# Optimization experiments

Hardware: AMD Instinct MI355X
Metric: run time of the kernel (lower is better)

The kernel has to match this reference:

```python
import jax, jax.numpy as jnp
import numpy as np

SIZES = (32, 64, 128, 256, 512)
RATIOS = (0.5, 1.0, 2.0)
STRIDE = 4
H = W = 256
IMG = 1024.0
NMS_THRESH = 0.7
MIN_SIZE = 1.0
BBOX_XFORM_CLIP = float(np.log(1000.0 / 16.0))
NEG = -1e9


def _make_anchors():
    # generate_anchors: ratio-major, scale-minor ordering, centered, rounded
    scales = np.asarray(SIZES, np.float32)
    ratios = np.asarray(RATIOS, np.float32)
    h_r = np.sqrt(ratios)
    w_r = 1.0 / h_r
    ws = (w_r[:, None] * scales[None, :]).reshape(-1)
    hs = (h_r[:, None] * scales[None, :]).reshape(-1)
    base = np.round(np.stack([-ws, -hs, ws, hs], axis=1) / 2.0)  # [A,4]
    # grid_anchors: (y,x)-major shifts, anchors innermost
    sx = np.arange(W, dtype=np.float32) * STRIDE
    sy = np.arange(H, dtype=np.float32) * STRIDE
    yy, xx = np.meshgrid(sy, sx, indexing="ij")
    shifts = np.stack([xx.ravel(), yy.ravel(), xx.ravel(), yy.ravel()], 1)  # [H*W,4]
    return (shifts[:, None, :] + base[None, :, :]).reshape(-1, 4).astype(np.float32)


def setup_inputs() -> dict:
    key = jax.random.key(0)
    k1, k2 = jax.random.split(key)
    N, A = 8, len(SIZES) * len(RATIOS)
    objectness = jax.random.normal(k1, (N, A, H, W), jnp.float32)
    box_regression = jax.random.normal(k2, (N, A * 4, H, W), jnp.float32) * 0.5
    anchors = jnp.asarray(_make_anchors())  # [H*W*A, 4]
    return {"objectness": objectness, "box_regression": box_regression,
            "anchors": anchors, "pre_nms_top_n": 2000}


def _decode(deltas, anchors):
    # BoxCoder.decode_single with weights (1,1,1,1)
    w = anchors[:, 2] - anchors[:, 0]
    h = anchors[:, 3] - anchors[:, 1]
    cx = anchors[:, 0] + 0.5 * w
    cy = anchors[:, 1] + 0.5 * h
    dx, dy = deltas[:, 0], deltas[:, 1]
    dw = jnp.minimum(deltas[:, 2], BBOX_XFORM_CLIP)
    dh = jnp.minimum(deltas[:, 3], BBOX_XFORM_CLIP)
    pcx = dx * w + cx
    pcy = dy * h + cy
    pw = jnp.exp(dw) * w
    ph = jnp.exp(dh) * h
    return jnp.stack([pcx - 0.5 * pw, pcy - 0.5 * ph,
                      pcx + 0.5 * pw, pcy + 0.5 * ph], axis=1)


def _nms_keep(boxes, thresh):
    # boxes [K,4] sorted by descending score; greedy NMS via fixed fori_loop
    x1, y1, x2, y2 = boxes[:, 0], boxes[:, 1], boxes[:, 2], boxes[:, 3]
    area = (x2 - x1) * (y2 - y1)
    lt = jnp.maximum(boxes[:, None, :2], boxes[None, :, :2])
    rb = jnp.minimum(boxes[:, None, 2:], boxes[None, :, 2:])
    wh = jnp.clip(rb - lt, 0.0)
    inter = wh[..., 0] * wh[..., 1]
    iou = inter / (area[:, None] + area[None, :] - inter)
    K = boxes.shape[0]
    rng = jnp.arange(K)

    def body(i, keep):
        sup = keep[i] & (iou[i] > thresh) & (rng > i)
        return keep & ~sup

    return jax.lax.fori_loop(0, K, body, jnp.ones((K,), bool))


def reference(objectness, box_regression, anchors, pre_nms_top_n):
    N, A, Hf, Wf = objectness.shape
    # permute_and_flatten: [N,A,H,W] -> [N, H*W*A] (h,w-major, anchor-minor)
    scores = objectness.transpose(0, 2, 3, 1).reshape(N, -1)
    deltas = (box_regression.reshape(N, A, 4, Hf, Wf)
              .transpose(0, 3, 4, 1, 2).reshape(N, -1, 4))
    proposals = jax.vmap(lambda d: _decode(d, anchors))(deltas)  # [N,M,4]
    # clip_boxes_to_image
    bx = jnp.clip(proposals[..., 0::2], 0.0, IMG)
    by = jnp.clip(proposals[..., 1::2], 0.0, IMG)
    proposals = jnp.stack([bx[..., 0], by[..., 0], bx[..., 1], by[..., 1]], -1)
    probs = jax.nn.sigmoid(scores)
    # remove_small_boxes (mask with -inf score instead of dynamic filter)
    valid = ((proposals[..., 2] - proposals[..., 0]) >= MIN_SIZE) & \
            ((proposals[..., 3] - proposals[..., 1]) >= MIN_SIZE)
    probs = jnp.where(valid, probs, NEG)
    top_scores, top_idx = jax.lax.top_k(probs, pre_nms_top_n)  # [N,K]
    top_boxes = jnp.take_along_axis(proposals, top_idx[..., None], axis=1)
    keep = jax.vmap(lambda b: _nms_keep(b, NMS_THRESH))(top_boxes)  # [N,K] bool
    kf = keep.astype(top_boxes.dtype)
    return jnp.concatenate([top_boxes * kf[..., None],
                            (top_scores * kf)[..., None]], axis=-1)  # [N,K,5]
```

## Files before the change

kernel.cpp:

```cpp
#include <hip/hip_runtime.h>
#include <stdint.h>

#define N_    8
#define A_    15
#define H_    256
#define W_    256
#define M_    (A_*H_*W_)
#define BINS  8192
#define BSH   19
#define KMAJ  3200
#define CAP   8192
#define CBUF  2048
#define WPR   32

__device__ __constant__ double CLIP_  = 4.135166556742356;
__device__ __constant__ double IMG_   = 1024.0;
__device__ __constant__ double MINSZ_ = 1.0;
__device__ __constant__ double NMST_  = 0.7;

__device__ __forceinline__ uint32_t ord32(float s) {
    uint32_t u = __float_as_uint(s);
    return u ^ (uint32_t)(((int32_t)u >> 31) | 0x80000000u);
}

__device__ __forceinline__ void decode_box(
    const float* __restrict__ breg, const float* __restrict__ anchors,
    int n, int a, int hw, int m,
    double& x1, double& y1, double& x2, double& y2)
{
    size_t bbase = ((size_t)(n*60 + a*4)) * 65536 + (size_t)hw;
    double d0 = (double)breg[bbase];
    double d1 = (double)breg[bbase + 65536];
    double d2 = (double)breg[bbase + 2*65536];
    double d3 = (double)breg[bbase + 3*65536];
    float4 av = *reinterpret_cast<const float4*>(anchors + (size_t)m*4);
    double a0 = (double)av.x, a1 = (double)av.y, a2 = (double)av.z, a3 = (double)av.w;
    double ww = a2 - a0, hh = a3 - a1;
    double cx = a0 + 0.5*ww, cy = a1 + 0.5*hh;
    double dw = fmin(d2, CLIP_), dh = fmin(d3, CLIP_);
    double pcx = d0*ww + cx, pcy = d1*hh + cy;
    double pw = exp(dw)*ww, ph = exp(dh)*hh;
    x1 = pcx - 0.5*pw; y1 = pcy - 0.5*ph;
    x2 = pcx + 0.5*pw; y2 = pcy + 0.5*ph;
    x1 = fmin(fmax(x1, 0.0), IMG_);
    y1 = fmin(fmax(y1, 0.0), IMG_);
    x2 = fmin(fmax(x2, 0.0), IMG_);
    y2 = fmin(fmax(y2, 0.0), IMG_);
}

__global__ void k_hist(const float* __restrict__ obj, unsigned int* __restrict__ hist)
{
    __shared__ unsigned int lh[BINS];
    const int n = blockIdx.y;
    for (int i = threadIdx.x; i < BINS; i += blockDim.x) lh[i] = 0;
    __syncthreads();
    const float4* objq = (const float4*)(obj + (size_t)n * M_);
    for (int it = 0; it < 32; ++it) {
        int q = blockIdx.x * 8192 + it * 256 + threadIdx.x;
        float4 v = objq[q];
        atomicAdd(&lh[ord32(v.x) >> BSH], 1u);
        atomicAdd(&lh[ord32(v.y) >> BSH], 1u);
        atomicAdd(&lh[ord32(v.z) >> BSH], 1u);
        atomicAdd(&lh[ord32(v.w) >> BSH], 1u);
    }
    __syncthreads();
    for (int i = threadIdx.x; i < BINS; i += blockDim.x) {
        unsigned int c = lh[i];
        if (c) atomicAdd(&hist[n*BINS + i], c);
    }
}

__global__ void k_findT(const unsigned int* __restrict__ hist, unsigned int* __restrict__ T)
{
    __shared__ unsigned int csum[256];
    const int n = blockIdx.x;
    const int tid = threadIdx.x;
    unsigned int s = 0;
    int hi = BINS - 1 - tid*32;
    for (int i = 0; i < 32; ++i) s += hist[n*BINS + hi - i];
    csum[tid] = s;
    __syncthreads();
    if (tid == 0) {
        unsigned int cum = 0; int c = 0;
        for (; c < 256; ++c) { if (cum + csum[c] >= (unsigned)KMAJ) break; cum += csum[c]; }
        if (c == 256) { T[n] = 0; return; }
        int hi2 = BINS - 1 - c*32;
        unsigned int cum2 = cum; int b = hi2;
        for (int i = 0; i < 32; ++i) {
            b = hi2 - i;
            cum2 += hist[n*BINS + b];
            if (cum2 >= (unsigned)KMAJ) break;
        }
        if (cum2 > (unsigned)CAP && b < BINS-1) b = b + 1;
        T[n] = (unsigned int)b;
    }
}

__global__ void k_collect(const float* __restrict__ obj, const float* __restrict__ breg,
                          const float* __restrict__ anchors, const unsigned int* __restrict__ T,
                          unsigned int* __restrict__ cnt, uint64_t* __restrict__ cand)
{
    __shared__ uint64_t buf[CBUF];
    __shared__ unsigned int lcnt, gbase;
    const int n = blockIdx.y;
    const unsigned int Tn = T[n];
    if (threadIdx.x == 0) lcnt = 0;
    __syncthreads();
    const float4* objq = (const float4*)(obj + (size_t)n * M_);
    for (int it = 0; it < 32; ++it) {
        int q = blockIdx.x * 8192 + it * 256 + threadIdx.x;
        float4 v = objq[q];
        int a = q >> 14;
        int hwq = q & 16383;
        #pragma unroll
        for (int e = 0; e < 4; ++e) {
            float s = (e==0) ? v.x : (e==1) ? v.y : (e==2) ? v.z : v.w;
            unsigned int o = ord32(s);
            if ((o >> BSH) < Tn) continue;
            int hw = hwq*4 + e;
            int m = hw*15 + a;
            double x1,y1,x2,y2;
            decode_box(breg, anchors, n, a, hw, m, x1,y1,x2,y2);
            if (!((x2 - x1 >= MINSZ_) && (y2 - y1 >= MINSZ_))) continue;
            uint64_t key = ((uint64_t)o << 32) | (uint32_t)(~(uint32_t)m);
            unsigned int p = atomicAdd(&lcnt, 1u);
            if (p < CBUF) buf[p] = key;
            else {
                unsigned int g = atomicAdd(&cnt[n*32], 1u);
                if (g < CAP) cand[(size_t)n*CAP + g] = key;
            }
        }
    }
    __syncthreads();
    if (threadIdx.x == 0) {
        unsigned int c = min(lcnt, (unsigned int)CBUF);
        gbase = atomicAdd(&cnt[n*32], c);
    }
    __syncthreads();
    unsigned int c = min(lcnt, (unsigned int)CBUF);
    for (unsigned int i = threadIdx.x; i < c; i += 256) {
        unsigned int g = gbase + i;
        if (g < CAP) cand[(size_t)n*CAP + g] = buf[i];
    }
}

__global__ void k_sort1k(uint64_t* __restrict__ cand, const unsigned int* __restrict__ cnt)
{
    __shared__ uint64_t s[1024];
    const int n = blockIdx.y, c = blockIdx.x;
    unsigned int cn = cnt[n*32]; if (cn > CAP) cn = CAP;
    uint64_t* base = cand + (size_t)n*CAP + c*1024;
    const int rem = (int)cn - c*1024;
    for (int i = threadIdx.x; i < 1024; i += blockDim.x)
        s[i] = (i < rem) ? base[i] : 0ull;
    __syncthreads();
    for (int k = 2; k <= 1024; k <<= 1) {
        for (int j = k >> 1; j > 0; j >>= 1) {
            for (int i = threadIdx.x; i < 1024; i += blockDim.x) {
                int l = i ^ j;
                if (l > i) {
                    uint64_t A = s[i], B = s[l];
                    bool up = ((i & k) == 0);
                    if ((A < B) == up) { s[i] = B; s[l] = A; }
                }
            }
            __syncthreads();
        }
    }
    for (int i = threadIdx.x; i < 1024; i += blockDim.x)
        base[i] = s[i];
}

__global__ void k_merge1(const uint64_t* __restrict__ cand, uint64_t* __restrict__ runs1)
{
    __shared__ uint64_t s[2048];
    const int n = blockIdx.y, jb = blockIdx.x;
    const uint64_t* A = cand + (size_t)n*CAP + (2*jb)*1024;
    const uint64_t* B = cand + (size_t)n*CAP + (2*jb+1)*1024;
    for (int i = threadIdx.x; i < 1024; i += blockDim.x) {
        uint64_t a = A[i], b = B[1023 - i];
        s[i]        = (a > b) ? a : b;
        s[i + 1024] = (a > b) ? b : a;
    }
    __syncthreads();
    for (int j = 512; j > 0; j >>= 1) {
        for (int i = threadIdx.x; i < 2048; i += blockDim.x) {
            int l = i ^ j;
            if (l > i) {
                uint64_t A2 = s[i], B2 = s[l];
                if (A2 < B2) { s[i] = B2; s[l] = A2; }
            }
        }
        __syncthreads();
    }
    uint64_t* dst = runs1 + ((size_t)n*4 + jb)*2048;
    for (int i = threadIdx.x; i < 2048; i += blockDim.x)
        dst[i] = s[i];
}

__device__ __forceinline__ void trunc_merge_body(
    const uint64_t* __restrict__ A, const uint64_t* __restrict__ B, uint64_t* s)
{
    for (int i = threadIdx.x; i < 2048; i += blockDim.x) {
        uint64_t a = A[i], b = B[2047 - i];
        s[i] = (a > b) ? a : b;
    }
    __syncthreads();
    for (int j = 1024; j > 0; j >>= 1) {
        for (int i = threadIdx.x; i < 2048; i += blockDim.x) {
            int l = i ^ j;
            if (l > i) {
                uint64_t A2 = s[i], B2 = s[l];
                if (A2 < B2) { s[i] = B2; s[l] = A2; }
            }
        }
        __syncthreads();
    }
}

__global__ void k_merge2(const uint64_t* __restrict__ runs1, uint64_t* __restrict__ runs2)
{
    __shared__ uint64_t s[2048];
    const int n = blockIdx.y, jb = blockIdx.x;
    trunc_merge_body(runs1 + ((size_t)n*4 + 2*jb)*2048,
                     runs1 + ((size_t)n*4 + 2*jb + 1)*2048, s);
    uint64_t* dst = runs2 + ((size_t)n*2 + jb)*2048;
    for (int i = threadIdx.x; i < 2048; i += blockDim.x)
        dst[i] = s[i];
}

__global__ void k_merge3_decode(const uint64_t* __restrict__ runs2,
                                const float* __restrict__ obj,
                                const float* __restrict__ breg,
                                const float* __restrict__ anchors,
                                double* __restrict__ boxes, double* __restrict__ probs,
                                int K)
{
    __shared__ uint64_t s[2048];
    const int n = blockIdx.x;
    trunc_merge_body(runs2 + ((size_t)n*2)*2048,
                     runs2 + ((size_t)n*2 + 1)*2048, s);
    for (int i = threadIdx.x; i < K; i += blockDim.x) {
        unsigned int m = ~((uint32_t)s[i]);
        int t = n*K + i;
        if (m >= (unsigned int)M_) {
            boxes[(size_t)t*4+0]=0.0; boxes[(size_t)t*4+1]=0.0;
            boxes[(size_t)t*4+2]=0.0; boxes[(size_t)t*4+3]=0.0;
            probs[t] = -1000000000.0;
            continue;
        }
        int a = (int)(m % 15u);
        int hw = (int)(m / 15u);
        double x1,y1,x2,y2;
        decode_box(breg, anchors, n, a, hw, (int)m, x1,y1,x2,y2);
        double* bx = boxes + (size_t)t*4;
        bx[0]=x1; bx[1]=y1; bx[2]=x2; bx[3]=y2;
        float sc = obj[((size_t)(n*15 + a)) * 65536 + hw];
        probs[t] = 1.0 / (1.0 + exp(-(double)sc));
    }
}

__global__ void k_sup(const double* __restrict__ boxes, uint64_t* __restrict__ sup, int K)
{
    __shared__ double jb[128][5];
    const int n = blockIdx.y;
    const int ntiles = (K + 127) >> 7;
    int p = blockIdx.x, ti = 0, rem = ntiles;
    while (p >= rem) { p -= rem; ++ti; --rem; }
    const int tj = ti + p;

    const int rowsj = min(128, K - tj*128);
    for (int x = threadIdx.x; x < rowsj*4; x += 256)
        jb[x >> 2][x & 3] = boxes[(((size_t)n*K) + tj*128)*4 + x];
    __syncthreads();
    if (threadIdx.x < (unsigned)rowsj)
        jb[threadIdx.x][4] = (jb[threadIdx.x][2]-jb[threadIdx.x][0]) *
                             (jb[threadIdx.x][3]-jb[threadIdx.x][1]);
    __syncthreads();

    const int il = threadIdx.x >> 1;
    const int word = threadIdx.x & 1;
    const int i = ti*128 + il;
    if (i >= K) return;

    const double* bi = boxes + (((size_t)n*K) + i)*4;
    double ix1=bi[0], iy1=bi[1], ix2=bi[2], iy2=bi[3];
    double ai = (ix2-ix1)*(iy2-iy1);

    uint64_t bits = 0;
    const int jb0 = word*64;
    const int jlim = min(rowsj - jb0, 64);
    const int jg0 = tj*128 + jb0;
    for (int b = 0; b < jlim; ++b) {
        int j = jg0 + b;
        if (j <= i) continue;
        double jx1=jb[jb0+b][0], jy1=jb[jb0+b][1], jx2=jb[jb0+b][2], jy2=jb[jb0+b][3];
        double aj = jb[jb0+b][4];
        double lx = fmax(ix1, jx1), ly = fmax(iy1, jy1);
        double rx = fmin(ix2, jx2), ry = fmin(iy2, jy2);
        double wx = fmax(rx - lx, 0.0), wy = fmax(ry - ly, 0.0);
        double inter = wx * wy;
        double iou = inter / (ai + aj - inter);
        if (iou > NMST_) bits |= (1ull << b);
    }
    sup[(((size_t)n*K) + i)*WPR + (tj*2 + word)] = bits;
}

__global__ void __launch_bounds__(256) k_nms_out(
    const uint64_t* __restrict__ sup, const double* __restrict__ boxes,
    const double* __restrict__ probs, float* __restrict__ out, int K)
{
    __shared__ uint64_t buf[2][64][WPR+1];
    __shared__ uint64_t keep_lds[WPR];
    const int n = blockIdx.x;
    const int tid = threadIdx.x;
    const int nch = (K + 63) >> 6;

    uint64_t keepw = 0;
    if (tid < WPR) {
        int base = tid * 64;
        if (base + 64 <= K) keepw = ~0ull;
        else if (base < K)  keepw = (~0ull) >> (64 - (K - base));
    }

    {
        const int tot = min(64, K) * WPR;
        const uint64_t* src = sup + ((size_t)n*K)*WPR;
        uint64_t tmp[8];
        #pragma unroll
        for (int k = 0; k < 8; ++k) {
            int x = tid + 256*k;
            tmp[k] = (x < tot) ? src[x] : 0ull;
        }
        #pragma unroll
        for (int k = 0; k < 8; ++k) {
            int x = tid + 256*k;
            if (x < tot) buf[0][x >> 5][x & 31] = tmp[k];
        }
    }
    __syncthreads();

    for (int c = 0; c < nch; ++c) {
        const int cur = c & 1;
        if (tid >= 64 && c + 1 < nch) {
            const int c1 = c + 1;
            const int i0 = c1 * 64;
            const int rows = min(64, K - i0);
            const uint64_t* src = sup + (((size_t)n*K) + i0)*WPR;
            const int t = tid - 64;
            const int lane_w = t & 31;
            const int rg = t >> 5;
            const int w = c1 + lane_w;
            uint64_t tmp[11];
            #pragma unroll
            for (int k = 0; k < 11; ++k) {
                int row = rg + 6*k;
                bool p = (w < WPR) && (row < rows);
                tmp[k] = p ? src[(size_t)row*WPR + w] : 0ull;
            }
            #pragma unroll
            for (int k = 0; k < 11; ++k) {
                int row = rg + 6*k;
                if ((w < WPR) && (row < rows)) buf[cur ^ 1][row][w] = tmp[k];
            }
        }
        if (tid < 64) {
            uint64_t diag = buf[cur][tid][c];
            uint32_t dlo = (uint32_t)diag;
            uint32_t dhi = (uint32_t)(diag >> 32);
            uint32_t alo = (uint32_t)__builtin_amdgcn_readlane((uint32_t)keepw, c);
            uint32_t ahi = (uint32_t)__builtin_amdgcn_readlane((uint32_t)(keepw >> 32), c);
            uint64_t alive = ((uint64_t)ahi << 32) | (uint64_t)alo;
            #pragma unroll
            for (int r = 0; r < 64; ++r) {
                uint64_t row =
                    ((uint64_t)(uint32_t)__builtin_amdgcn_readlane(dhi, r) << 32)
                  |  (uint64_t)(uint32_t)__builtin_amdgcn_readlane(dlo, r);
                uint64_t msk = (uint64_t)0 - ((alive >> r) & 1ull);
                alive &= ~(row & msk);
            }
            if (tid == c) keepw = alive;
            const int w = tid & 31;
            const int r0 = (tid >> 5) * 32;
            uint64_t pend = 0;
            #pragma unroll
            for (int rr = 0; rr < 32; ++rr) {
                int r = r0 + rr;
                uint64_t msk = (uint64_t)0 - ((alive >> r) & 1ull);
                pend |= buf[cur][r][w] & msk;
            }
            pend |= (uint64_t)__shfl_xor((unsigned long long)pend, 32, 64);
            if (tid < WPR && tid > c) keepw &= ~pend;
        }
        __syncthreads();
    }

    if (tid < WPR) keep_lds[tid] = keepw;
    __syncthreads();

    for (int k = tid; k < K; k += 256) {
        uint64_t w = keep_lds[k >> 6];
        double f = ((w >> (k & 63)) & 1ull) ? 1.0 : 0.0;
        const double* b = boxes + (((size_t)n*K) + k)*4;
        float* o = out + (((size_t)n*K) + k)*5;
        o[0] = (float)(b[0]*f);
        o[1] = (float)(b[1]*f);
        o[2] = (float)(b[2]*f);
        o[3] = (float)(b[3]*f);
        o[4] = (float)(probs[(size_t)n*K + k]*f);
    }
}

extern "C" void kernel_launch(void* const* d_in, const int* in_sizes, int n_in,
                              void* d_out, int out_size, void* d_ws, size_t ws_size,
                              hipStream_t stream)
{
    const float* obj     = (const float*)d_in[0];
    const float* breg    = (const float*)d_in[1];
    const float* anchors = (const float*)d_in[2];
    float* out = (float*)d_out;

    const int K = out_size / (N_ * 5);

    char* ws = (char*)d_ws;
    unsigned int* hist  = (unsigned int*)(ws + 0);
    unsigned int* T     = (unsigned int*)(ws + 262144);
    unsigned int* cnt   = (unsigned int*)(ws + 262272);
    double*       boxes = (double*)      (ws + 327680);
    double*       probs = (double*)      (ws + 839680);
    uint64_t*     sup   = (uint64_t*)    (ws + 970752);
    uint64_t*     cand  = (uint64_t*)    (ws + 970752);
    uint64_t*     runs1 = (uint64_t*)    (ws + 970752 + 524288);
    uint64_t*     runs2 = (uint64_t*)    (ws + 970752 + 1048576);

    hipMemsetAsync(ws, 0, 263296, stream);

    dim3 gH(30, N_);
    k_hist<<<gH, 256, 0, stream>>>(obj, hist);
    k_findT<<<N_, 256, 0, stream>>>(hist, T);
    k_collect<<<gH, 256, 0, stream>>>(obj, breg, anchors, T, cnt, cand);
    k_sort1k<<<dim3(8, N_), 512, 0, stream>>>(cand, cnt);
    k_merge1<<<dim3(4, N_), 1024, 0, stream>>>(cand, runs1);
    k_merge2<<<dim3(2, N_), 1024, 0, stream>>>(runs1, runs2);
    k_merge3_decode<<<N_, 1024, 0, stream>>>(runs2, obj, breg, anchors, boxes, probs, K);
    const int ntiles = (K + 127) >> 7;
    dim3 gS(ntiles*(ntiles+1)/2, N_);
    k_sup<<<gS, 256, 0, stream>>>(boxes, sup, K);
    k_nms_out<<<N_, 256, 0, stream>>>(sup, boxes, probs, out, K);
}
```

Measured before the change: 227.7 us.

## Process NMS suppression mask in 128-row chunks with swizzled LDS layout

The serial NMS reduction kernel now handles two 64-bit keep words per chunk iteration instead of one. This halves the number of chunk iterations and block barriers. LDS padding is replaced by an XOR-free rotate swizzle ((w+row)&31) to avoid bank conflicts, and the separate keep array is folded into the buffer. In exchange, each iteration carries a longer serial readlane chain and uses more registers for prefetch staging.

```diff
diff --git a/kernel.cpp b/kernel.cpp
--- a/kernel.cpp
+++ b/kernel.cpp
@@ -12,6 +12,7 @@
 #define CAP   8192
 #define CBUF  2048
 #define WPR   32
+#define CH    128
 
 __device__ __constant__ double CLIP_  = 4.135166556742356;
 __device__ __constant__ double IMG_   = 1024.0;
@@ -310,11 +311,10 @@
     const uint64_t* __restrict__ sup, const double* __restrict__ boxes,
     const double* __restrict__ probs, float* __restrict__ out, int K)
 {
-    __shared__ uint64_t buf[2][64][WPR+1];
-    __shared__ uint64_t keep_lds[WPR];
+    __shared__ uint64_t buf[2][CH][WPR];
     const int n = blockIdx.x;
     const int tid = threadIdx.x;
-    const int nch = (K + 63) >> 6;
+    const int nch = (K + CH - 1) >> 7;
 
     uint64_t keepw = 0;
     if (tid < WPR) {
@@ -324,82 +324,107 @@
     }
 
     {
-        const int tot = min(64, K) * WPR;
+        const int rows = min(CH, K);
+        const int tot = rows * WPR;
         const uint64_t* src = sup + ((size_t)n*K)*WPR;
-        uint64_t tmp[8];
+        uint64_t tmp[16];
         #pragma unroll
-        for (int k = 0; k < 8; ++k) {
+        for (int k = 0; k < 16; ++k) {
             int x = tid + 256*k;
             tmp[k] = (x < tot) ? src[x] : 0ull;
         }
         #pragma unroll
-        for (int k = 0; k < 8; ++k) {
+        for (int k = 0; k < 16; ++k) {
             int x = tid + 256*k;
-            if (x < tot) buf[0][x >> 5][x & 31] = tmp[k];
+            if (x < tot) {
+                int row = x >> 5, w = x & 31;
+                buf[0][row][(w + row) & 31] = tmp[k];
+            }
         }
     }
     __syncthreads();
 
     for (int c = 0; c < nch; ++c) {
         const int cur = c & 1;
+        const int w0 = 2 * c;
         if (tid >= 64 && c + 1 < nch) {
             const int c1 = c + 1;
-            const int i0 = c1 * 64;
-            const int rows = min(64, K - i0);
+            const int i0 = c1 * CH;
+            const int rows = min(CH, K - i0);
             const uint64_t* src = sup + (((size_t)n*K) + i0)*WPR;
             const int t = tid - 64;
-            const int lane_w = t & 31;
+            const int w = 2*c1 + (t & 31);
             const int rg = t >> 5;
-            const int w = c1 + lane_w;
-            uint64_t tmp[11];
+            uint64_t tmp[22];
             #pragma unroll
-            for (int k = 0; k < 11; ++k) {
+            for (int k = 0; k < 22; ++k) {
                 int row = rg + 6*k;
                 bool p = (w < WPR) && (row < rows);
                 tmp[k] = p ? src[(size_t)row*WPR + w] : 0ull;
             }
             #pragma unroll
-            for (int k = 0; k < 11; ++k) {
+            for (int k = 0; k < 22; ++k) {
                 int row = rg + 6*k;
-                if ((w < WPR) && (row < rows)) buf[cur ^ 1][row][w] = tmp[k];
+                if ((w < WPR) && (row < rows))
+                    buf[cur ^ 1][row][(w + row) & 31] = tmp[k];
             }
         }
         if (tid < 64) {
-            uint64_t diag = buf[cur][tid][c];
-            uint32_t dlo = (uint32_t)diag;
-            uint32_t dhi = (uint32_t)(diag >> 32);
-            uint32_t alo = (uint32_t)__builtin_amdgcn_readlane((uint32_t)keepw, c);
-            uint32_t ahi = (uint32_t)__builtin_amdgcn_readlane((uint32_t)(keepw >> 32), c);
-            uint64_t alive = ((uint64_t)ahi << 32) | (uint64_t)alo;
+            uint64_t d0 = buf[cur][tid]     [(w0     + tid) & 31];
+            uint64_t d1 = buf[cur][tid]     [(w0 + 1 + tid) & 31];
+            uint64_t e1 = buf[cur][64 + tid][(w0 + 1 + tid) & 31];
+            uint32_t d0lo = (uint32_t)d0, d0hi = (uint32_t)(d0 >> 32);
+            uint32_t d1lo = (uint32_t)d1, d1hi = (uint32_t)(d1 >> 32);
+            uint32_t e1lo = (uint32_t)e1, e1hi = (uint32_t)(e1 >> 32);
+            uint32_t alo0 = (uint32_t)__builtin_amdgcn_readlane((uint32_t)keepw, w0);
+            uint32_t ahi0 = (uint32_t)__builtin_amdgcn_readlane((uint32_t)(keepw >> 32), w0);
+            uint32_t alo1 = (uint32_t)__builtin_amdgcn_readlane((uint32_t)keepw, w0 + 1);
+            uint32_t ahi1 = (uint32_t)__builtin_amdgcn_readlane((uint32_t)(keepw >> 32), w0 + 1);
+            uint64_t a0 = ((uint64_t)ahi0 << 32) | (uint64_t)alo0;
+            uint64_t a1 = ((uint64_t)ahi1 << 32) | (uint64_t)alo1;
             #pragma unroll
             for (int r = 0; r < 64; ++r) {
-                uint64_t row =
-                    ((uint64_t)(uint32_t)__builtin_amdgcn_readlane(dhi, r) << 32)
-                  |  (uint64_t)(uint32_t)__builtin_amdgcn_readlane(dlo, r);
-                uint64_t msk = (uint64_t)0 - ((alive >> r) & 1ull);
-                alive &= ~(row & msk);
-            }
-            if (tid == c) keepw = alive;
+                uint64_t r0 =
+                    ((uint64_t)(uint32_t)__builtin_amdgcn_readlane(d0hi, r) << 32)
+                  |  (uint64_t)(uint32_t)__builtin_amdgcn_readlane(d0lo, r);
+                uint64_t r1 =
+                    ((uint64_t)(uint32_t)__builtin_amdgcn_readlane(d1hi, r) << 32)
+                  |  (uint64_t)(uint32_t)__builtin_amdgcn_readlane(d1lo, r);
+                uint64_t msk = (uint64_t)0 - ((a0 >> r) & 1ull);
+                a0 &= ~(r0 & msk);
+                a1 &= ~(r1 & msk);
+            }
+            #pragma unroll
+            for (int r = 0; r < 64; ++r) {
+                uint64_t r1 =
+                    ((uint64_t)(uint32_t)__builtin_amdgcn_readlane(e1hi, r) << 32)
+                  |  (uint64_t)(uint32_t)__builtin_amdgcn_readlane(e1lo, r);
+                uint64_t msk = (uint64_t)0 - ((a1 >> r) & 1ull);
+                a1 &= ~(r1 & msk);
+            }
+            if (tid == w0)     keepw = a0;
+            if (tid == w0 + 1) keepw = a1;
             const int w = tid & 31;
-            const int r0 = (tid >> 5) * 32;
+            const int rbase = (tid >> 5) * 64;
+            const uint64_t sel = (tid & 32) ? a1 : a0;
             uint64_t pend = 0;
             #pragma unroll
-            for (int rr = 0; rr < 32; ++rr) {
-                int r = r0 + rr;
-                uint64_t msk = (uint64_t)0 - ((alive >> r) & 1ull);
-                pend |= buf[cur][r][w] & msk;
+            for (int rr = 0; rr < 64; ++rr) {
+                int row = rbase + rr;
+                uint64_t msk = (uint64_t)0 - ((sel >> rr) & 1ull);
+                pend |= buf[cur][row][(w + row) & 31] & msk;
             }
             pend |= (uint64_t)__shfl_xor((unsigned long long)pend, 32, 64);
-            if (tid < WPR && tid > c) keepw &= ~pend;
+            if (tid < WPR && tid > w0 + 1) keepw &= ~pend;
         }
         __syncthreads();
     }
 
-    if (tid < WPR) keep_lds[tid] = keepw;
+    if (tid < WPR) buf[0][0][tid] = keepw;
     __syncthreads();
 
     for (int k = tid; k < K; k += 256) {
-        uint64_t w = keep_lds[k >> 6];
+        uint64_t w = buf[0][0][k >> 6];
         double f = ((w >> (k & 63)) & 1ull) ? 1.0 : 0.0;
         const double* b = boxes + (((size_t)n*K) + k)*4;
         float* o = out + (((size_t)n*K) + k)*5;
```

Result: slower. 232.5 us (+2.1%).
